# Kernel optimization log

Measured on AMD Instinct MI355X. Metric: run time of the kernel, lower is better.

The kernel has to match this reference:

```python
import jax, jax.numpy as jnp
import numpy as np

IN_FEATS, N_HIDDEN, NUM_LAYERS, N_CLASSES, CLS_HIDDEN = 166, 76, 2, 2, 510
T, N, E = 3, 100000, 1600000
RRELU_SLOPE = (1.0 / 8.0 + 1.0 / 3.0) / 2.0  # eval-mode RReLU = leaky relu with mean slope


def setup_inputs() -> dict:
    key = jax.random.key(0)
    ks = jax.random.split(key, 24)
    d = {}
    d['feats'] = jax.random.normal(ks[0], (T, N, IN_FEATS), jnp.float32)
    d['src'] = jax.random.randint(ks[1], (T, E), 0, N, jnp.int32)
    d['dst'] = jax.random.randint(ks[2], (T, E), 0, N, jnp.int32)
    # TopK scorers (uniform +-1/sqrt(feats))
    s0 = 1.0 / np.sqrt(IN_FEATS)
    s1 = 1.0 / np.sqrt(N_HIDDEN)
    d['scorer0'] = jax.random.uniform(ks[3], (IN_FEATS, 1), jnp.float32, -s0, s0)
    d['scorer1'] = jax.random.uniform(ks[4], (N_HIDDEN, 1), jnp.float32, -s1, s1)
    # GCN weights (xavier-ish)
    d['gcn_w0'] = jax.random.normal(ks[5], (IN_FEATS, N_HIDDEN), jnp.float32) * np.sqrt(2.0 / (IN_FEATS + N_HIDDEN))
    d['gcn_w1'] = jax.random.normal(ks[6], (N_HIDDEN, N_HIDDEN), jnp.float32) * np.sqrt(2.0 / (2 * N_HIDDEN))
    # GRU params, torch layout: W_ih [3H, H_in], W_hh [3H, H], gate order (r, z, n)
    g = 1.0 / np.sqrt(N_HIDDEN)
    H3 = 3 * N_HIDDEN
    d['gru0_wih'] = jax.random.uniform(ks[7], (H3, N_HIDDEN), jnp.float32, -g, g)
    d['gru0_whh'] = jax.random.uniform(ks[8], (H3, N_HIDDEN), jnp.float32, -g, g)
    d['gru0_bih'] = jax.random.uniform(ks[9], (H3,), jnp.float32, -g, g)
    d['gru0_bhh'] = jax.random.uniform(ks[10], (H3,), jnp.float32, -g, g)
    d['gru1_wih'] = jax.random.uniform(ks[11], (H3, N_HIDDEN), jnp.float32, -g, g)
    d['gru1_whh'] = jax.random.uniform(ks[12], (H3, N_HIDDEN), jnp.float32, -g, g)
    d['gru1_bih'] = jax.random.uniform(ks[13], (H3,), jnp.float32, -g, g)
    d['gru1_bhh'] = jax.random.uniform(ks[14], (H3,), jnp.float32, -g, g)
    # MLP
    m1 = 1.0 / np.sqrt(N_HIDDEN)
    m2 = 1.0 / np.sqrt(CLS_HIDDEN)
    d['mlp_w1'] = jax.random.uniform(ks[15], (N_HIDDEN, CLS_HIDDEN), jnp.float32, -m1, m1)
    d['mlp_b1'] = jax.random.uniform(ks[16], (CLS_HIDDEN,), jnp.float32, -m1, m1)
    d['mlp_w2'] = jax.random.uniform(ks[17], (CLS_HIDDEN, N_CLASSES), jnp.float32, -m2, m2)
    d['mlp_b2'] = jax.random.uniform(ks[18], (N_CLASSES,), jnp.float32, -m2, m2)
    return d


def _topk_pool(x, scorer, k):
    # x: [N, F]; returns X_tilde: [F, k]
    scores = (x @ scorer).ravel() / jnp.linalg.norm(scorer)
    vals, idx = jax.lax.top_k(scores, k)
    out = x[idx] * jnp.tanh(vals)[:, None]  # [k, F]
    return out.T


def _gru_step(x, h, wih, whh, bih, bhh):
    # x: [B, H_in], h: [B, H]; torch GRU gate order r, z, n
    gx = x @ wih.T + bih
    gh = h @ whh.T + bhh
    H = h.shape[1]
    rx, zx, nx = gx[:, :H], gx[:, H:2 * H], gx[:, 2 * H:]
    rh, zh, nh = gh[:, :H], gh[:, H:2 * H], gh[:, 2 * H:]
    r = jax.nn.sigmoid(rx + rh)
    z = jax.nn.sigmoid(zx + zh)
    n = jnp.tanh(nx + r * nh)
    return (1.0 - z) * n + z * h


def _graph_conv(x, W, src, dst, n_nodes):
    # DGL GraphConv, norm='both', bias=False, RReLU (eval) activation
    deg_out = jnp.zeros((n_nodes,), x.dtype).at[src].add(1.0)
    deg_in = jnp.zeros((n_nodes,), x.dtype).at[dst].add(1.0)
    norm_src = jnp.clip(deg_out, 1.0, None) ** -0.5
    norm_dst = jnp.clip(deg_in, 1.0, None) ** -0.5
    h = (x * norm_src[:, None]) @ W  # project first (small out dim)
    agg = jax.ops.segment_sum(h[src], dst, num_segments=n_nodes)
    out = agg * norm_dst[:, None]
    return jnp.where(out >= 0, out, out * RRELU_SLOPE)


def reference(feats, src, dst, scorer0, scorer1, gcn_w0, gcn_w1,
              gru0_wih, gru0_whh, gru0_bih, gru0_bhh,
              gru1_wih, gru1_whh, gru1_bih, gru1_bhh,
              mlp_w1, mlp_b1, mlp_w2, mlp_b2):
    scorers = [scorer0, scorer1]
    gcn_ws = [gcn_w0, gcn_w1]
    grus = [(gru0_wih, gru0_whh, gru0_bih, gru0_bhh),
            (gru1_wih, gru1_whh, gru1_bih, gru1_bhh)]
    feat_list = [feats[t] for t in range(T)]
    for i in range(NUM_LAYERS):
        W = gcn_ws[i]
        wih, whh, bih, bhh = grus[i]
        for t in range(T):
            x_tilde = _topk_pool(feat_list[t], scorers[i], N_HIDDEN)  # [F, k]
            W = _gru_step(x_tilde, W, wih, whh, bih, bhh)  # evolve weights
            feat_list[t] = _graph_conv(feat_list[t], W, src[t], dst[t], N)
    h = feat_list[-1]
    h = jax.nn.relu(h @ mlp_w1 + mlp_b1)
    return h @ mlp_w2 + mlp_b2
```

## Files before the change

kernel.cpp:

```cpp
#include <hip/hip_runtime.h>
#include <math.h>

#define NN 100000
#define EE 1600000
#define F0 166
#define HID 76
#define H3 228
#define CHID 510
#define SLOPE 0.22916666666666666f
#define CAND_MAX 4096
#define NBIN 4096
#define HPAD 20

#define BSH 9
#define BSZ 512
#define NBKT 196
#define CH 4096
#define NCHK 391

__device__ __forceinline__ unsigned f2key(float f){
    unsigned u = __float_as_uint(f);
    return (u & 0x80000000u) ? ~u : (u | 0x80000000u);
}
__device__ __forceinline__ float key2f(unsigned k){
    unsigned u = (k & 0x80000000u) ? (k & 0x7fffffffu) : ~k;
    return __uint_as_float(u);
}

__global__ void scorer_norms_k(const float* __restrict__ s0, const float* __restrict__ s1,
                               float* __restrict__ outn){
    __shared__ float red[256];
    int tid = threadIdx.x;
    float a = 0.f;
    for (int k = tid; k < F0; k += 256) a += s0[k]*s0[k];
    red[tid] = a; __syncthreads();
    for (int s = 128; s > 0; s >>= 1){ if (tid < s) red[tid] += red[tid+s]; __syncthreads(); }
    if (tid == 0) outn[0] = 1.0f/sqrtf(red[0]);
    __syncthreads();
    float b = 0.f;
    for (int k = tid; k < HID; k += 256) b += s1[k]*s1[k];
    red[tid] = b; __syncthreads();
    for (int s = 128; s > 0; s >>= 1){ if (tid < s) red[tid] += red[tid+s]; __syncthreads(); }
    if (tid == 0) outn[1] = 1.0f/sqrtf(red[0]);
}

__global__ void pad_k(const float* __restrict__ w1, const float* __restrict__ b1,
                      const float* __restrict__ w2, float* __restrict__ w1t,
                      float* __restrict__ b1p, float* __restrict__ w2p){
    int idx = blockIdx.x*256 + threadIdx.x;
    if (idx < 512*HID){
        int j = idx / HID, k = idx - j*HID;
        w1t[idx] = (j < CHID) ? w1[k*CHID + j] : 0.f;
    }
    if (idx < 512)  b1p[idx] = (idx < CHID)   ? b1[idx] : 0.f;
    if (idx < 1024) w2p[idx] = (idx < CHID*2) ? w2[idx] : 0.f;
}


__global__ __launch_bounds__(256) void p1_hist_k(const int* __restrict__ src, const int* __restrict__ dst,
                                                 int* __restrict__ bhS, int* __restrict__ bhD){
    __shared__ int hS[NBKT], hD[NBKT];
    int t = blockIdx.y, blk = blockIdx.x, tid = threadIdx.x;
    for (int i = tid; i < NBKT; i += 256){ hS[i] = 0; hD[i] = 0; }
    __syncthreads();
    size_t ebase = (size_t)t*EE + (size_t)blk*CH;
    int m = EE - blk*CH; if (m > CH) m = CH;
    for (int j = tid; j < m; j += 256){
        atomicAdd(&hS[src[ebase + j] >> BSH], 1);
        atomicAdd(&hD[dst[ebase + j] >> BSH], 1);
    }
    __syncthreads();
    for (int i = tid; i < NBKT; i += 256){
        bhS[((size_t)t*NBKT + i)*NCHK + blk] = hS[i];
        bhD[((size_t)t*NBKT + i)*NCHK + blk] = hD[i];
    }
}

__global__ __launch_bounds__(512) void p2_scan_k(int* __restrict__ bhS, int* __restrict__ bhD,
                                                 int* __restrict__ ctS, int* __restrict__ ctD){
    __shared__ int sd[512];
    int b = blockIdx.x, t = blockIdx.y, tid = threadIdx.x;
    for (int a = 0; a < 2; a++){
        int* bh = a ? bhD : bhS;
        int* ct = a ? ctD : ctS;
        int* row = bh + ((size_t)t*NBKT + b)*NCHK;
        int v = (tid < NCHK) ? row[tid] : 0;
        sd[tid] = v; __syncthreads();
        for (int off = 1; off < 512; off <<= 1){
            int x = (tid >= off) ? sd[tid - off] : 0;
            __syncthreads();
            sd[tid] += x;
            __syncthreads();
        }
        if (tid < NCHK) row[tid] = sd[tid] - v;
        if (tid == 511) ct[t*NBKT + b] = sd[511];
        __syncthreads();
    }
}

__global__ __launch_bounds__(256) void p3_base_k(const int* __restrict__ ctS, const int* __restrict__ ctD,
                                                 int* __restrict__ bbS, int* __restrict__ bbD){
    __shared__ int sd[256];
    int tid = threadIdx.x;
    for (int a = 0; a < 2; a++){
        const int* ct = a ? ctD : ctS;
        int* bb = a ? bbD : bbS;
        for (int t = 0; t < 3; t++){
            int v = (tid < NBKT) ? ct[t*NBKT + tid] : 0;
            sd[tid] = v; __syncthreads();
            for (int off = 1; off < 256; off <<= 1){
                int x = (tid >= off) ? sd[tid - off] : 0;
                __syncthreads();
                sd[tid] += x;
                __syncthreads();
            }
            if (tid < NBKT) bb[t*(NBKT+1) + tid] = sd[tid] - v;
            if (tid == 0)   bb[t*(NBKT+1) + NBKT] = EE;
            __syncthreads();
        }
    }
}

__global__ __launch_bounds__(256) void p4_scatter_k(const int* __restrict__ src, const int* __restrict__ dst,
                                                    const int* __restrict__ bhS, const int* __restrict__ bhD,
                                                    const int* __restrict__ bbS, const int* __restrict__ bbD,
                                                    int* __restrict__ srcpart,
                                                    unsigned long long* __restrict__ pairpart){
    __shared__ int baseS[NBKT], baseD[NBKT], cS[NBKT], cD[NBKT];
    int t = blockIdx.y, blk = blockIdx.x, tid = threadIdx.x;
    for (int i = tid; i < NBKT; i += 256){
        baseS[i] = bbS[t*(NBKT+1) + i] + bhS[((size_t)t*NBKT + i)*NCHK + blk];
        baseD[i] = bbD[t*(NBKT+1) + i] + bhD[((size_t)t*NBKT + i)*NCHK + blk];
        cS[i] = 0; cD[i] = 0;
    }
    __syncthreads();
    size_t ebase = (size_t)t*EE + (size_t)blk*CH;
    int m = EE - blk*CH; if (m > CH) m = CH;
    int* sp = srcpart + (size_t)t*EE;
    unsigned long long* pp = pairpart + (size_t)t*EE;
    for (int j = tid; j < m; j += 256){
        int s = src[ebase + j], d = dst[ebase + j];
        int bs = s >> BSH, bd = d >> BSH;
        int r0 = atomicAdd(&cS[bs], 1);
        sp[baseS[bs] + r0] = s;
        int r1 = atomicAdd(&cD[bd], 1);
        pp[baseD[bd] + r1] = ((unsigned long long)(unsigned)s << 32) | (unsigned)d;
    }
}

__global__ __launch_bounds__(256) void p5_degO_k(const int* __restrict__ srcpart,
                                                 const int* __restrict__ bbS,
                                                 int* __restrict__ degO){
    __shared__ int cnt[BSZ];
    int b = blockIdx.x, t = blockIdx.y, tid = threadIdx.x;
    for (int i = tid; i < BSZ; i += 256) cnt[i] = 0;
    __syncthreads();
    int st = bbS[t*(NBKT+1) + b], en = bbS[t*(NBKT+1) + b + 1];
    const int* sp = srcpart + (size_t)t*EE;
    for (int j = st + tid; j < en; j += 256) atomicAdd(&cnt[sp[j] & (BSZ-1)], 1);
    __syncthreads();
    int nb = b << BSH;
    for (int i = tid; i < BSZ; i += 256){
        int n = nb + i;
        if (n < NN) degO[t*NN + n] = cnt[i];
    }
}

__global__ __launch_bounds__(512) void p6_csr_k(const unsigned long long* __restrict__ pairpart,
                                                const int* __restrict__ bbD,
                                                int* __restrict__ degI, int* __restrict__ rs,
                                                int* __restrict__ col){
    __shared__ int cnt[BSZ];
    __shared__ int sc[BSZ];
    __shared__ int fc[BSZ];
    int b = blockIdx.x, t = blockIdx.y, tid = threadIdx.x;
    cnt[tid] = 0; fc[tid] = 0;
    __syncthreads();
    int st = bbD[t*(NBKT+1) + b], en = bbD[t*(NBKT+1) + b + 1];
    const unsigned long long* pp = pairpart + (size_t)t*EE;
    for (int j = st + tid; j < en; j += 512)
        atomicAdd(&cnt[(int)(pp[j] & (unsigned long long)(BSZ-1))], 1);
    __syncthreads();
    int v = cnt[tid];
    sc[tid] = v; __syncthreads();
    for (int off = 1; off < 512; off <<= 1){
        int x = (tid >= off) ? sc[tid - off] : 0;
        __syncthreads();
        sc[tid] += x;
        __syncthreads();
    }
    int ex = sc[tid] - v;
    int nb = b << BSH;
    int n = nb + tid;
    if (n < NN){ degI[t*NN + n] = v; rs[t*NN + n] = st + ex; }
    sc[tid] = ex;
    __syncthreads();
    int* ct = col + (size_t)t*EE;
    for (int j = st + tid; j < en; j += 512){
        unsigned long long p = pp[j];
        int d = (int)(p & 0xffffffffull);
        int li = d & (BSZ-1);
        int r = atomicAdd(&fc[li], 1);
        ct[st + sc[li] + r] = (int)(p >> 32);
    }
}


__global__ void norm_k(const int* __restrict__ degO, const int* __restrict__ degI,
                       float* __restrict__ nO, float* __restrict__ nI){
    int t = blockIdx.y;
    int n = blockIdx.x*256 + threadIdx.x;
    if (n < NN){
        int o = degO[t*NN + n]; if (o < 1) o = 1;
        int i = degI[t*NN + n]; if (i < 1) i = 1;
        nO[t*NN + n] = 1.0f/sqrtf((float)o);
        nI[t*NN + n] = 1.0f/sqrtf((float)i);
    }
}

template<int F, int PAD>
__global__ __launch_bounds__(256) void score_k(const float* __restrict__ x,
                                               const float* __restrict__ scorer,
                                               const float* __restrict__ invn,
                                               float* __restrict__ scores,
                                               unsigned* hist){
    __shared__ float xs[64*PAD];
    __shared__ float part[256];
    int tid = threadIdx.x;
    int n0 = blockIdx.x*64;
    int nodes = NN - n0; if (nodes > 64) nodes = 64;
    for (int idx = tid; idx < nodes*F; idx += 256){
        int n = idx / F, k = idx - n*F;
        xs[n*PAD + k] = x[(size_t)(n0+n)*F + k];
    }
    __syncthreads();
    int w = __builtin_amdgcn_readfirstlane(tid >> 6);
    int lane = tid & 63;
    int k0 = (F*w) >> 2, k1 = (F*(w+1)) >> 2;
    const float* xrow = xs + lane*PAD;
    float s = 0.f;
    for (int k = k0; k < k1; k++) s += xrow[k]*scorer[k];
    part[w*64 + lane] = s;
    __syncthreads();
    if (tid < 64 && n0 + tid < NN){
        float tot = (part[tid] + part[64+tid] + part[128+tid] + part[192+tid]) * invn[0];
        scores[n0 + tid] = tot;
        atomicAdd(&hist[f2key(tot) >> 20], 1u);
    }
}

__global__ void select_bin_k(const unsigned* __restrict__ hist, int* thr){
    __shared__ unsigned cs[256];
    int tid = threadIdx.x;
    unsigned s = 0;
    int base = NBIN - 1 - tid*16;
    for (int j = 0; j < 16; j++) s += hist[base - j];
    cs[tid] = s; __syncthreads();
    if (tid == 0){
        unsigned acc = 0; int c = 0;
        for (; c < 256; c++){ if (acc + cs[c] >= 76u) break; acc += cs[c]; }
        int b = NBIN - 1 - c*16;
        int sel = 0;
        for (int j = 0; j < 16; j++){
            acc += hist[b - j];
            if (acc >= 76u){ sel = b - j; break; }
        }
        *thr = sel;
    }
}

__global__ void compact_k(const float* __restrict__ scores, const int* __restrict__ thr,
                          float* __restrict__ cv, int* __restrict__ ci, int* cnt){
    int n = blockIdx.x*256 + threadIdx.x;
    if (n >= NN) return;
    float s = scores[n];
    if ((int)(f2key(s) >> 20) >= *thr){
        int p = atomicAdd(cnt, 1);
        if (p < CAND_MAX){ cv[p] = s; ci[p] = n; }
    }
}

__global__ __launch_bounds__(256) void topk_k(const float* __restrict__ cv,
                                              const int* __restrict__ ci,
                                              const int* __restrict__ cnt,
                                              int* __restrict__ topidx,
                                              float* __restrict__ tanhv){
    __shared__ unsigned long long keys[CAND_MAX];
    int tid = threadIdx.x;
    int M = *cnt; if (M > CAND_MAX) M = CAND_MAX;
    for (int i = tid; i < M; i += 256)
        keys[i] = ((unsigned long long)f2key(cv[i]) << 32) | (unsigned)(~ci[i]);
    __syncthreads();
    for (int i = tid; i < M; i += 256){
        unsigned long long ki = keys[i];
        int r = 0;
        for (int j = 0; j < M; j++) r += (keys[j] > ki) ? 1 : 0;
        if (r < 76){
            topidx[r] = (int)(~(unsigned)(ki & 0xffffffffu));
            tanhv[r]  = tanhf(key2f((unsigned)(ki >> 32)));
        }
    }
}

template<int F>
__global__ void gru_k(const float* __restrict__ cur, const int* __restrict__ topidx,
                      const float* __restrict__ tanhv, float* __restrict__ W,
                      float* __restrict__ Wt,
                      const float* __restrict__ wih, const float* __restrict__ whh,
                      const float* __restrict__ bih, const float* __restrict__ bhh){
    __shared__ float xr[HID], hr[HID], gx[H3], gh[H3];
    int r = blockIdx.x, tid = threadIdx.x;
    if (tid < HID){
        xr[tid] = cur[(size_t)topidx[tid]*F + r] * tanhv[tid];
        hr[tid] = W[r*HID + tid];
    }
    __syncthreads();
    if (tid < H3){
        const float* wi = wih + tid*HID;
        const float* wh = whh + tid*HID;
        float sa = 0.f, sb = 0.f;
        for (int k = 0; k < HID; k++){ sa += xr[k]*wi[k]; sb += hr[k]*wh[k]; }
        gx[tid] = bih[tid] + sa;
        gh[tid] = bhh[tid] + sb;
    }
    __syncthreads();
    if (tid < HID){
        float rr = 1.f/(1.f + expf(-(gx[tid] + gh[tid])));
        float zz = 1.f/(1.f + expf(-(gx[HID+tid] + gh[HID+tid])));
        float nn = tanhf(gx[2*HID+tid] + rr*gh[2*HID+tid]);
        float nv = (1.f - zz)*nn + zz*hr[tid];
        W[r*HID + tid] = nv;
        int c = tid >> 2, i = tid & 3;
        Wt[(c*F + r)*4 + i] = nv;
    }
}

template<int F, int PAD, int NB>
__global__ __launch_bounds__(256) void gemm_k(const float* __restrict__ x,
                                              const float* __restrict__ Wt,
                                              const float* __restrict__ nO,
                                              float* __restrict__ h){
    __shared__ __align__(16) float xs[NB*PAD];
    int tid = threadIdx.x;
    int n0 = blockIdx.x*NB;
    int nodes = NN - n0; if (nodes > NB) nodes = NB;
    for (int idx = tid; idx < nodes*F; idx += 256){
        int n = idx / F, k = idx - n*F;
        xs[n*PAD + k] = x[(size_t)(n0+n)*F + k];
    }
    __syncthreads();
    int w = __builtin_amdgcn_readfirstlane(tid >> 6);
    int lane = tid & 63;
    int c0 = w*5;
    const float4* Wt4 = (const float4*)Wt;
    float4 accA[5], accB[5];
    #pragma unroll
    for (int c = 0; c < 5; c++){
        accA[c] = make_float4(0.f,0.f,0.f,0.f);
        accB[c] = make_float4(0.f,0.f,0.f,0.f);
    }
    const float* xA = xs + lane*PAD;
    const float* xB = xs + ((NB==128) ? (lane+64)*PAD : lane*PAD);
    for (int k = 0; k < F; k++){
        float xa = xA[k];
        float xb = 0.f;
        if constexpr (NB == 128) xb = xB[k];
        #pragma unroll
        for (int c = 0; c < 5; c++){
            float4 wv = Wt4[(c0 + c)*F + k];
            accA[c].x += xa*wv.x; accA[c].y += xa*wv.y;
            accA[c].z += xa*wv.z; accA[c].w += xa*wv.w;
            if constexpr (NB == 128){
                accB[c].x += xb*wv.x; accB[c].y += xb*wv.y;
                accB[c].z += xb*wv.z; accB[c].w += xb*wv.w;
            }
        }
    }
    int nc = (w == 3) ? 4 : 5;
    int nA = n0 + lane;
    if (nA < NN){
        float nm = nO[nA];
        float4* h4 = (float4*)h + (size_t)nA*HPAD + c0;
        for (int c = 0; c < nc; c++){
            float4 a = accA[c];
            h4[c] = make_float4(a.x*nm, a.y*nm, a.z*nm, a.w*nm);
        }
    }
    if constexpr (NB == 128){
        int nB = n0 + 64 + lane;
        if (nB < NN){
            float nm = nO[nB];
            float4* h4 = (float4*)h + (size_t)nB*HPAD + c0;
            for (int c = 0; c < nc; c++){
                float4 a = accB[c];
                h4[c] = make_float4(a.x*nm, a.y*nm, a.z*nm, a.w*nm);
            }
        }
    }
}

__global__ void agg_k(const int* __restrict__ rs, const int* __restrict__ degI,
                      const int* __restrict__ col, const float* __restrict__ h,
                      const float* __restrict__ nI, float* __restrict__ ft){
    int idx = blockIdx.x*256 + threadIdx.x;
    if (idx >= NN*19) return;
    int n = idx/19, c = idx - n*19;
    int st = rs[n], cnt = degI[n];
    const float4* h4 = (const float4*)h;
    float ax=0.f, ay=0.f, az=0.f, aw=0.f;
    int e = 0;
    for (; e + 2 <= cnt; e += 2){
        int s0 = col[st + e];
        int s1 = col[st + e + 1];
        float4 v0 = h4[(size_t)s0*HPAD + c];
        float4 v1 = h4[(size_t)s1*HPAD + c];
        ax += v0.x + v1.x; ay += v0.y + v1.y;
        az += v0.z + v1.z; aw += v0.w + v1.w;
    }
    if (e < cnt){
        int s = col[st + e];
        float4 v = h4[(size_t)s*HPAD + c];
        ax += v.x; ay += v.y; az += v.z; aw += v.w;
    }
    float nm = nI[n];
    ax*=nm; ay*=nm; az*=nm; aw*=nm;
    ax = ax >= 0.f ? ax : ax*SLOPE;
    ay = ay >= 0.f ? ay : ay*SLOPE;
    az = az >= 0.f ? az : az*SLOPE;
    aw = aw >= 0.f ? aw : aw*SLOPE;
    ((float4*)ft)[(size_t)n*19 + c] = make_float4(ax,ay,az,aw);
}

__global__ __launch_bounds__(256) void mlp_k(const float* __restrict__ ft,
                                             const float* __restrict__ w1t,
                                             const float* __restrict__ b1p,
                                             const float* __restrict__ w2p,
                                             const float* __restrict__ b2,
                                             float* __restrict__ out){
    __shared__ __align__(16) float hs[128*HID];
    __shared__ float apA0[256], apA1[256], apB0[256], apB1[256];
    int tid = threadIdx.x;
    int n0 = blockIdx.x*128;
    int nodes = NN - n0; if (nodes > 128) nodes = 128;
    const float4* g4 = (const float4*)(ft + (size_t)n0*HID);
    float4* s4 = (float4*)hs;
    int lim = nodes*19;
    for (int idx = tid; idx < 128*19; idx += 256)
        s4[idx] = (idx < lim) ? g4[idx] : make_float4(0.f,0.f,0.f,0.f);
    __syncthreads();
    int w = __builtin_amdgcn_readfirstlane(tid >> 6);
    int lane = tid & 63;
    const float4* hA = (const float4*)(hs + lane*HID);
    const float4* hB = (const float4*)(hs + (lane+64)*HID);
    float aA0=0.f, aA1=0.f, aB0=0.f, aB1=0.f;
    for (int g = w; g < 128; g += 4){
        int j0 = g << 2;
        const float* wr = w1t + j0*HID;
        float b0 = b1p[j0], b1v = b1p[j0+1], b2v = b1p[j0+2], b3v = b1p[j0+3];
        float sA0=b0, sA1=b1v, sA2=b2v, sA3=b3v;
        float sB0=b0, sB1=b1v, sB2=b2v, sB3=b3v;
        #pragma unroll
        for (int k4 = 0; k4 < 19; k4++){
            float4 a = hA[k4];
            float4 b = hB[k4];
            int k = k4 << 2;
            float w00=wr[k],         w01=wr[k+1],         w02=wr[k+2],         w03=wr[k+3];
            float w10=wr[HID+k],     w11=wr[HID+k+1],     w12=wr[HID+k+2],     w13=wr[HID+k+3];
            float w20=wr[2*HID+k],   w21=wr[2*HID+k+1],   w22=wr[2*HID+k+2],   w23=wr[2*HID+k+3];
            float w30=wr[3*HID+k],   w31=wr[3*HID+k+1],   w32=wr[3*HID+k+2],   w33=wr[3*HID+k+3];
            sA0 += a.x*w00 + a.y*w01 + a.z*w02 + a.w*w03;
            sA1 += a.x*w10 + a.y*w11 + a.z*w12 + a.w*w13;
            sA2 += a.x*w20 + a.y*w21 + a.z*w22 + a.w*w23;
            sA3 += a.x*w30 + a.y*w31 + a.z*w32 + a.w*w33;
            sB0 += b.x*w00 + b.y*w01 + b.z*w02 + b.w*w03;
            sB1 += b.x*w10 + b.y*w11 + b.z*w12 + b.w*w13;
            sB2 += b.x*w20 + b.y*w21 + b.z*w22 + b.w*w23;
            sB3 += b.x*w30 + b.y*w31 + b.z*w32 + b.w*w33;
        }
        sA0 = fmaxf(sA0, 0.f); sA1 = fmaxf(sA1, 0.f);
        sA2 = fmaxf(sA2, 0.f); sA3 = fmaxf(sA3, 0.f);
        sB0 = fmaxf(sB0, 0.f); sB1 = fmaxf(sB1, 0.f);
        sB2 = fmaxf(sB2, 0.f); sB3 = fmaxf(sB3, 0.f);
        float u00 = w2p[j0*2],   u01 = w2p[j0*2+1];
        float u10 = w2p[j0*2+2], u11 = w2p[j0*2+3];
        float u20 = w2p[j0*2+4], u21 = w2p[j0*2+5];
        float u30 = w2p[j0*2+6], u31 = w2p[j0*2+7];
        aA0 += sA0*u00 + sA1*u10 + sA2*u20 + sA3*u30;
        aA1 += sA0*u01 + sA1*u11 + sA2*u21 + sA3*u31;
        aB0 += sB0*u00 + sB1*u10 + sB2*u20 + sB3*u30;
        aB1 += sB0*u01 + sB1*u11 + sB2*u21 + sB3*u31;
    }
    apA0[w*64 + lane] = aA0; apA1[w*64 + lane] = aA1;
    apB0[w*64 + lane] = aB0; apB1[w*64 + lane] = aB1;
    __syncthreads();
    if (tid < 64){
        int n = n0 + tid;
        if (n < NN){
            float r0 = apA0[tid] + apA0[64+tid] + apA0[128+tid] + apA0[192+tid] + b2[0];
            float r1 = apA1[tid] + apA1[64+tid] + apA1[128+tid] + apA1[192+tid] + b2[1];
            out[(size_t)n*2]   = r0;
            out[(size_t)n*2+1] = r1;
        }
    } else if (tid < 128){
        int l = tid - 64;
        int n = n0 + 64 + l;
        if (n < NN){
            float r0 = apB0[l] + apB0[64+l] + apB0[128+l] + apB0[192+l] + b2[0];
            float r1 = apB1[l] + apB1[64+l] + apB1[128+l] + apB1[192+l] + b2[1];
            out[(size_t)n*2]   = r0;
            out[(size_t)n*2+1] = r1;
        }
    }
}

extern "C" void kernel_launch(void* const* d_in, const int* in_sizes, int n_in,
                              void* d_out, int out_size, void* d_ws, size_t ws_size,
                              hipStream_t stream)
{
    (void)in_sizes; (void)n_in; (void)out_size; (void)ws_size;
    const float* feats   = (const float*)d_in[0];
    const int*   src     = (const int*)d_in[1];
    const int*   dst     = (const int*)d_in[2];
    const float* scorer0 = (const float*)d_in[3];
    const float* scorer1 = (const float*)d_in[4];
    const float* gcnw[2] = {(const float*)d_in[5],  (const float*)d_in[6]};
    const float* wih[2]  = {(const float*)d_in[7],  (const float*)d_in[11]};
    const float* whh[2]  = {(const float*)d_in[8],  (const float*)d_in[12]};
    const float* bih[2]  = {(const float*)d_in[9],  (const float*)d_in[13]};
    const float* bhh[2]  = {(const float*)d_in[10], (const float*)d_in[14]};
    const float* w1 = (const float*)d_in[15];
    const float* b1 = (const float*)d_in[16];
    const float* w2 = (const float*)d_in[17];
    const float* b2 = (const float*)d_in[18];
    float* out = (float*)d_out;

    char* p = (char*)d_ws;
    auto alloc = [&](size_t bytes) -> void* {
        void* r = (void*)p;
        p += (bytes + 255) & ~(size_t)255;
        return r;
    };
    float* ft[3];
    for (int t = 0; t < 3; t++) ft[t] = (float*)alloc((size_t)NN*HID*4);
    float* hbuf    = (float*)alloc((size_t)NN*HPAD*16);
    int*   col_all = (int*)alloc((size_t)3*EE*4);
    float* nO_all  = (float*)alloc((size_t)3*NN*4);
    float* nI_all  = (float*)alloc((size_t)3*NN*4);
    int*   rs_all  = (int*)alloc((size_t)3*NN*4);
    int*   dO_all  = (int*)alloc((size_t)3*NN*4);
    int*   dI_all  = (int*)alloc((size_t)3*NN*4);
    int* srcpart = (int*)alloc((size_t)3*EE*4);
    unsigned long long* pairpart = (unsigned long long*)alloc((size_t)3*EE*8);
    int* bhS = (int*)alloc((size_t)3*NBKT*NCHK*4);
    int* bhD = (int*)alloc((size_t)3*NBKT*NCHK*4);
    int* ctS = (int*)alloc((size_t)3*NBKT*4);
    int* ctD = (int*)alloc((size_t)3*NBKT*4);
    int* bbS = (int*)alloc((size_t)3*(NBKT+1)*4);
    int* bbD = (int*)alloc((size_t)3*(NBKT+1)*4);

    float*    scores = (float*)alloc((size_t)NN*4);
    float*    cv     = (float*)alloc(CAND_MAX*4);
    int*      ci     = (int*)alloc(CAND_MAX*4);
    int*      thr    = (int*)alloc(256);
    int*      topidx = (int*)alloc(128*4);
    float*    tanhv  = (float*)alloc(128*4);
    float*    Wbuf   = (float*)alloc((size_t)F0*HID*4 + 256);
    float*    Wt     = (float*)alloc((size_t)19*F0*16 + 4096);
    float*    invn   = (float*)alloc(256);
    float*    w1t    = (float*)alloc((size_t)512*HID*4);
    float*    b1p    = (float*)alloc(512*4);
    float*    w2p    = (float*)alloc(1024*4);

    char* zbase = p;
    unsigned* hist6 = (unsigned*)alloc((size_t)6*NBIN*4);
    int*      ccnt6 = (int*)alloc(6*256);
    size_t zsize = (size_t)(p - zbase);

    const int gN  = (NN + 255)/256;
    const int gA  = (NN*19 + 255)/256;
    const int gB  = (NN + 63)/64;
    const int gB2 = (NN + 127)/128;
    const int gP  = (512*HID + 255)/256;

    hipMemsetAsync(zbase, 0, zsize, stream);
    scorer_norms_k<<<1,256,0,stream>>>(scorer0, scorer1, invn);
    pad_k<<<gP,256,0,stream>>>(w1, b1, w2, w1t, b1p, w2p);

    p1_hist_k<<<dim3(NCHK,3),256,0,stream>>>(src, dst, bhS, bhD);
    p2_scan_k<<<dim3(NBKT,3),512,0,stream>>>(bhS, bhD, ctS, ctD);
    p3_base_k<<<1,256,0,stream>>>(ctS, ctD, bbS, bbD);
    p4_scatter_k<<<dim3(NCHK,3),256,0,stream>>>(src, dst, bhS, bhD, bbS, bbD, srcpart, pairpart);
    p5_degO_k<<<dim3(NBKT,3),256,0,stream>>>(srcpart, bbS, dO_all);
    p6_csr_k<<<dim3(NBKT,3),512,0,stream>>>(pairpart, bbD, dI_all, rs_all, col_all);
    norm_k<<<dim3(gN,3),256,0,stream>>>(dO_all, dI_all, nO_all, nI_all);

    for (int i = 0; i < 2; i++){
        hipMemcpyAsync(Wbuf, gcnw[i], (size_t)((i==0)?F0:HID)*HID*4, hipMemcpyDeviceToDevice, stream);
        for (int t = 0; t < 3; t++){
            int q = i*3 + t;
            unsigned* hist = hist6 + (size_t)q*NBIN;
            int* ccnt = ccnt6 + q*64;
            const float* cur = (i == 0) ? (feats + (size_t)t*NN*F0) : ft[t];
            if (i == 0) score_k<F0,167><<<gB,256,0,stream>>>(cur, scorer0, invn+0, scores, hist);
            else        score_k<HID,77><<<gB,256,0,stream>>>(cur, scorer1, invn+1, scores, hist);
            select_bin_k<<<1,256,0,stream>>>(hist, thr);
            compact_k<<<gN,256,0,stream>>>(scores, thr, cv, ci, ccnt);
            topk_k<<<1,256,0,stream>>>(cv, ci, ccnt, topidx, tanhv);
            if (i == 0){
                gru_k<F0><<<F0,256,0,stream>>>(cur, topidx, tanhv, Wbuf, Wt, wih[i], whh[i], bih[i], bhh[i]);
                gemm_k<F0,167,64><<<gB,256,0,stream>>>(cur, Wt, nO_all + (size_t)t*NN, hbuf);
            } else {
                gru_k<HID><<<HID,256,0,stream>>>(cur, topidx, tanhv, Wbuf, Wt, wih[i], whh[i], bih[i], bhh[i]);
                gemm_k<HID,77,128><<<gB2,256,0,stream>>>(cur, Wt, nO_all + (size_t)t*NN, hbuf);
            }
            agg_k<<<gA,256,0,stream>>>(rs_all + (size_t)t*NN, dI_all + (size_t)t*NN,
                                       col_all + (size_t)t*EE, hbuf, nI_all + (size_t)t*NN, ft[t]);
        }
    }

    mlp_k<<<gB2,256,0,stream>>>(ft[2], w1t, b1p, w2p, b2, out);
}
```

Measured before the change: 2.558 ms.

## Fuse norm and select kernels, unroll aggregation, restructure MLP with split-J atomics

Norm computation moves into the degree and CSR kernels, and threshold selection moves into every compact block, which removes two launches per stage. The aggregation gather loop is unrolled to four edges to keep more loads in flight. The MLP is rewritten so that each thread holds one node row in registers, W1 slices are staged in shared memory, and the hidden dimension is split across two blocks whose partial outputs are combined with atomics into a zeroed output. The MLP change adds register pressure, a memset, atomics and nondeterministic summation order, and every compact block now recomputes the histogram selection.

After: 2.587 ms. No clear change (+1.1%).

```diff
diff --git a/kernel.cpp b/kernel.cpp
--- a/kernel.cpp
+++ b/kernel.cpp
@@ -11,6 +11,7 @@
 #define CAND_MAX 4096
 #define NBIN 4096
 #define HPAD 20
+#define MJ 256
 
 #define BSH 9
 #define BSZ 512
@@ -150,7 +151,7 @@
 
 __global__ __launch_bounds__(256) void p5_degO_k(const int* __restrict__ srcpart,
                                                  const int* __restrict__ bbS,
-                                                 int* __restrict__ degO){
+                                                 float* __restrict__ nO){
     __shared__ int cnt[BSZ];
     int b = blockIdx.x, t = blockIdx.y, tid = threadIdx.x;
     for (int i = tid; i < BSZ; i += 256) cnt[i] = 0;
@@ -162,13 +163,17 @@
     int nb = b << BSH;
     for (int i = tid; i < BSZ; i += 256){
         int n = nb + i;
-        if (n < NN) degO[t*NN + n] = cnt[i];
+        if (n < NN){
+            int o = cnt[i]; if (o < 1) o = 1;
+            nO[t*NN + n] = 1.0f/sqrtf((float)o);
+        }
     }
 }
 
 __global__ __launch_bounds__(512) void p6_csr_k(const unsigned long long* __restrict__ pairpart,
                                                 const int* __restrict__ bbD,
                                                 int* __restrict__ degI, int* __restrict__ rs,
+                                                float* __restrict__ nI,
                                                 int* __restrict__ col){
     __shared__ int cnt[BSZ];
     __shared__ int sc[BSZ];
@@ -192,7 +197,12 @@
     int ex = sc[tid] - v;
     int nb = b << BSH;
     int n = nb + tid;
-    if (n < NN){ degI[t*NN + n] = v; rs[t*NN + n] = st + ex; }
+    if (n < NN){
+        degI[t*NN + n] = v;
+        rs[t*NN + n] = st + ex;
+        int ii = v; if (ii < 1) ii = 1;
+        nI[t*NN + n] = 1.0f/sqrtf((float)ii);
+    }
     sc[tid] = ex;
     __syncthreads();
     int* ct = col + (size_t)t*EE;
@@ -205,18 +215,6 @@
     }
 }
 
-
-__global__ void norm_k(const int* __restrict__ degO, const int* __restrict__ degI,
-                       float* __restrict__ nO, float* __restrict__ nI){
-    int t = blockIdx.y;
-    int n = blockIdx.x*256 + threadIdx.x;
-    if (n < NN){
-        int o = degO[t*NN + n]; if (o < 1) o = 1;
-        int i = degI[t*NN + n]; if (i < 1) i = 1;
-        nO[t*NN + n] = 1.0f/sqrtf((float)o);
-        nI[t*NN + n] = 1.0f/sqrtf((float)i);
-    }
-}
 
 template<int F, int PAD>
 __global__ __launch_bounds__(256) void score_k(const float* __restrict__ x,
@@ -249,8 +247,11 @@
     }
 }
 
-__global__ void select_bin_k(const unsigned* __restrict__ hist, int* thr){
+__global__ __launch_bounds__(256) void compact_k(const float* __restrict__ scores,
+                                                 const unsigned* __restrict__ hist,
+                                                 float* __restrict__ cv, int* __restrict__ ci, int* cnt){
     __shared__ unsigned cs[256];
+    __shared__ int thr_s;
     int tid = threadIdx.x;
     unsigned s = 0;
     int base = NBIN - 1 - tid*16;
@@ -265,18 +266,16 @@
             acc += hist[b - j];
             if (acc >= 76u){ sel = b - j; break; }
         }
-        *thr = sel;
-    }
-}
-
-__global__ void compact_k(const float* __restrict__ scores, const int* __restrict__ thr,
-                          float* __restrict__ cv, int* __restrict__ ci, int* cnt){
-    int n = blockIdx.x*256 + threadIdx.x;
+        thr_s = sel;
+    }
+    __syncthreads();
+    int thr = thr_s;
+    int n = blockIdx.x*256 + tid;
     if (n >= NN) return;
-    float s = scores[n];
-    if ((int)(f2key(s) >> 20) >= *thr){
+    float sv = scores[n];
+    if ((int)(f2key(sv) >> 20) >= thr){
         int p = atomicAdd(cnt, 1);
-        if (p < CAND_MAX){ cv[p] = s; ci[p] = n; }
+        if (p < CAND_MAX){ cv[p] = sv; ci[p] = n; }
     }
 }
 
@@ -409,15 +408,21 @@
     const float4* h4 = (const float4*)h;
     float ax=0.f, ay=0.f, az=0.f, aw=0.f;
     int e = 0;
-    for (; e + 2 <= cnt; e += 2){
+    for (; e + 4 <= cnt; e += 4){
         int s0 = col[st + e];
         int s1 = col[st + e + 1];
+        int s2 = col[st + e + 2];
+        int s3 = col[st + e + 3];
         float4 v0 = h4[(size_t)s0*HPAD + c];
         float4 v1 = h4[(size_t)s1*HPAD + c];
-        ax += v0.x + v1.x; ay += v0.y + v1.y;
-        az += v0.z + v1.z; aw += v0.w + v1.w;
-    }
-    if (e < cnt){
+        float4 v2 = h4[(size_t)s2*HPAD + c];
+        float4 v3 = h4[(size_t)s3*HPAD + c];
+        ax += (v0.x + v1.x) + (v2.x + v3.x);
+        ay += (v0.y + v1.y) + (v2.y + v3.y);
+        az += (v0.z + v1.z) + (v2.z + v3.z);
+        aw += (v0.w + v1.w) + (v2.w + v3.w);
+    }
+    for (; e < cnt; e++){
         int s = col[st + e];
         float4 v = h4[(size_t)s*HPAD + c];
         ax += v.x; ay += v.y; az += v.z; aw += v.w;
@@ -431,86 +436,55 @@
     ((float4*)ft)[(size_t)n*19 + c] = make_float4(ax,ay,az,aw);
 }
 
-__global__ __launch_bounds__(256) void mlp_k(const float* __restrict__ ft,
-                                             const float* __restrict__ w1t,
-                                             const float* __restrict__ b1p,
-                                             const float* __restrict__ w2p,
-                                             const float* __restrict__ b2,
-                                             float* __restrict__ out){
-    __shared__ __align__(16) float hs[128*HID];
-    __shared__ float apA0[256], apA1[256], apB0[256], apB1[256];
-    int tid = threadIdx.x;
-    int n0 = blockIdx.x*128;
-    int nodes = NN - n0; if (nodes > 128) nodes = 128;
-    const float4* g4 = (const float4*)(ft + (size_t)n0*HID);
-    float4* s4 = (float4*)hs;
-    int lim = nodes*19;
-    for (int idx = tid; idx < 128*19; idx += 256)
-        s4[idx] = (idx < lim) ? g4[idx] : make_float4(0.f,0.f,0.f,0.f);
-    __syncthreads();
-    int w = __builtin_amdgcn_readfirstlane(tid >> 6);
-    int lane = tid & 63;
-    const float4* hA = (const float4*)(hs + lane*HID);
-    const float4* hB = (const float4*)(hs + (lane+64)*HID);
-    float aA0=0.f, aA1=0.f, aB0=0.f, aB1=0.f;
-    for (int g = w; g < 128; g += 4){
-        int j0 = g << 2;
-        const float* wr = w1t + j0*HID;
-        float b0 = b1p[j0], b1v = b1p[j0+1], b2v = b1p[j0+2], b3v = b1p[j0+3];
-        float sA0=b0, sA1=b1v, sA2=b2v, sA3=b3v;
-        float sB0=b0, sB1=b1v, sB2=b2v, sB3=b3v;
+__global__ __launch_bounds__(1024) void mlp2_k(const float* __restrict__ ft,
+                                               const float* __restrict__ w1t,
+                                               const float* __restrict__ b1p,
+                                               const float* __restrict__ w2p,
+                                               const float* __restrict__ b2,
+                                               float* __restrict__ out){
+    __shared__ __align__(16) float ws[MJ*HID];
+    __shared__ float w2s[MJ*2];
+    __shared__ float b1s[MJ];
+    int tid = threadIdx.x;
+    int jbase = blockIdx.y * MJ;
+    const float4* wg = (const float4*)(w1t + (size_t)jbase*HID);
+    float4* wsv = (float4*)ws;
+    for (int i = tid; i < MJ*HID/4; i += 1024) wsv[i] = wg[i];
+    if (tid < MJ*2) w2s[tid] = w2p[jbase*2 + tid];
+    if (tid < MJ)   b1s[tid] = b1p[jbase + tid];
+    __syncthreads();
+    int node = blockIdx.x*1024 + tid;
+    if (node >= NN) return;
+    float4 r[19];
+    const float4* rp = (const float4*)(ft + (size_t)node*HID);
+    #pragma unroll
+    for (int k = 0; k < 19; k++) r[k] = rp[k];
+    float acc0 = 0.f, acc1 = 0.f;
+    if (jbase == 0){ acc0 = b2[0]; acc1 = b2[1]; }
+    const float4* ws4 = (const float4*)ws;
+    for (int g = 0; g < MJ/4; g++){
+        int j0 = g*4;
+        float s0 = b1s[j0], s1 = b1s[j0+1], s2 = b1s[j0+2], s3 = b1s[j0+3];
+        const float4* wr = ws4 + j0*19;
         #pragma unroll
         for (int k4 = 0; k4 < 19; k4++){
-            float4 a = hA[k4];
-            float4 b = hB[k4];
-            int k = k4 << 2;
-            float w00=wr[k],         w01=wr[k+1],         w02=wr[k+2],         w03=wr[k+3];
-            float w10=wr[HID+k],     w11=wr[HID+k+1],     w12=wr[HID+k+2],     w13=wr[HID+k+3];
-            float w20=wr[2*HID+k],   w21=wr[2*HID+k+1],   w22=wr[2*HID+k+2],   w23=wr[2*HID+k+3];
-            float w30=wr[3*HID+k],   w31=wr[3*HID+k+1],   w32=wr[3*HID+k+2],   w33=wr[3*HID+k+3];
-            sA0 += a.x*w00 + a.y*w01 + a.z*w02 + a.w*w03;
-            sA1 += a.x*w10 + a.y*w11 + a.z*w12 + a.w*w13;
-            sA2 += a.x*w20 + a.y*w21 + a.z*w22 + a.w*w23;
-            sA3 += a.x*w30 + a.y*w31 + a.z*w32 + a.w*w33;
-            sB0 += b.x*w00 + b.y*w01 + b.z*w02 + b.w*w03;
-            sB1 += b.x*w10 + b.y*w11 + b.z*w12 + b.w*w13;
-            sB2 += b.x*w20 + b.y*w21 + b.z*w22 + b.w*w23;
-            sB3 += b.x*w30 + b.y*w31 + b.z*w32 + b.w*w33;
-        }
-        sA0 = fmaxf(sA0, 0.f); sA1 = fmaxf(sA1, 0.f);
-        sA2 = fmaxf(sA2, 0.f); sA3 = fmaxf(sA3, 0.f);
-        sB0 = fmaxf(sB0, 0.f); sB1 = fmaxf(sB1, 0.f);
-        sB2 = fmaxf(sB2, 0.f); sB3 = fmaxf(sB3, 0.f);
-        float u00 = w2p[j0*2],   u01 = w2p[j0*2+1];
-        float u10 = w2p[j0*2+2], u11 = w2p[j0*2+3];
-        float u20 = w2p[j0*2+4], u21 = w2p[j0*2+5];
-        float u30 = w2p[j0*2+6], u31 = w2p[j0*2+7];
-        aA0 += sA0*u00 + sA1*u10 + sA2*u20 + sA3*u30;
-        aA1 += sA0*u01 + sA1*u11 + sA2*u21 + sA3*u31;
-        aB0 += sB0*u00 + sB1*u10 + sB2*u20 + sB3*u30;
-        aB1 += sB0*u01 + sB1*u11 + sB2*u21 + sB3*u31;
-    }
-    apA0[w*64 + lane] = aA0; apA1[w*64 + lane] = aA1;
-    apB0[w*64 + lane] = aB0; apB1[w*64 + lane] = aB1;
-    __syncthreads();
-    if (tid < 64){
-        int n = n0 + tid;
-        if (n < NN){
-            float r0 = apA0[tid] + apA0[64+tid] + apA0[128+tid] + apA0[192+tid] + b2[0];
-            float r1 = apA1[tid] + apA1[64+tid] + apA1[128+tid] + apA1[192+tid] + b2[1];
-            out[(size_t)n*2]   = r0;
-            out[(size_t)n*2+1] = r1;
-        }
-    } else if (tid < 128){
-        int l = tid - 64;
-        int n = n0 + 64 + l;
-        if (n < NN){
-            float r0 = apB0[l] + apB0[64+l] + apB0[128+l] + apB0[192+l] + b2[0];
-            float r1 = apB1[l] + apB1[64+l] + apB1[128+l] + apB1[192+l] + b2[1];
-            out[(size_t)n*2]   = r0;
-            out[(size_t)n*2+1] = r1;
-        }
-    }
+            float4 rv = r[k4];
+            float4 w0 = wr[k4];
+            float4 w1 = wr[19 + k4];
+            float4 w2v = wr[38 + k4];
+            float4 w3 = wr[57 + k4];
+            s0 += rv.x*w0.x + rv.y*w0.y + rv.z*w0.z + rv.w*w0.w;
+            s1 += rv.x*w1.x + rv.y*w1.y + rv.z*w1.z + rv.w*w1.w;
+            s2 += rv.x*w2v.x + rv.y*w2v.y + rv.z*w2v.z + rv.w*w2v.w;
+            s3 += rv.x*w3.x + rv.y*w3.y + rv.z*w3.z + rv.w*w3.w;
+        }
+        s0 = fmaxf(s0, 0.f); s1 = fmaxf(s1, 0.f);
+        s2 = fmaxf(s2, 0.f); s3 = fmaxf(s3, 0.f);
+        acc0 += s0*w2s[j0*2]   + s1*w2s[j0*2+2] + s2*w2s[j0*2+4] + s3*w2s[j0*2+6];
+        acc1 += s0*w2s[j0*2+1] + s1*w2s[j0*2+3] + s2*w2s[j0*2+5] + s3*w2s[j0*2+7];
+    }
+    atomicAdd(&out[(size_t)node*2],     acc0);
+    atomicAdd(&out[(size_t)node*2 + 1], acc1);
 }
 
 extern "C" void kernel_launch(void* const* d_in, const int* in_sizes, int n_in,
@@ -547,7 +521,6 @@
     float* nO_all  = (float*)alloc((size_t)3*NN*4);
     float* nI_all  = (float*)alloc((size_t)3*NN*4);
     int*   rs_all  = (int*)alloc((size_t)3*NN*4);
-    int*   dO_all  = (int*)alloc((size_t)3*NN*4);
     int*   dI_all  = (int*)alloc((size_t)3*NN*4);
     int* srcpart = (int*)alloc((size_t)3*EE*4);
     unsigned long long* pairpart = (unsigned long long*)alloc((size_t)3*EE*8);
@@ -561,7 +534,6 @@
     float*    scores = (float*)alloc((size_t)NN*4);
     float*    cv     = (float*)alloc(CAND_MAX*4);
     int*      ci     = (int*)alloc(CAND_MAX*4);
-    int*      thr    = (int*)alloc(256);
     int*      topidx = (int*)alloc(128*4);
     float*    tanhv  = (float*)alloc(128*4);
     float*    Wbuf   = (float*)alloc((size_t)F0*HID*4 + 256);
@@ -580,9 +552,11 @@
     const int gA  = (NN*19 + 255)/256;
     const int gB  = (NN + 63)/64;
     const int gB2 = (NN + 127)/128;
+    const int gM  = (NN + 1023)/1024;
     const int gP  = (512*HID + 255)/256;
 
     hipMemsetAsync(zbase, 0, zsize, stream);
+    hipMemsetAsync(out, 0, (size_t)NN*2*4, stream);
     scorer_norms_k<<<1,256,0,stream>>>(scorer0, scorer1, invn);
     pad_k<<<gP,256,0,stream>>>(w1, b1, w2, w1t, b1p, w2p);
 
@@ -590,9 +564,8 @@
     p2_scan_k<<<dim3(NBKT,3),512,0,stream>>>(bhS, bhD, ctS, ctD);
     p3_base_k<<<1,256,0,stream>>>(ctS, ctD, bbS, bbD);
     p4_scatter_k<<<dim3(NCHK,3),256,0,stream>>>(src, dst, bhS, bhD, bbS, bbD, srcpart, pairpart);
-    p5_degO_k<<<dim3(NBKT,3),256,0,stream>>>(srcpart, bbS, dO_all);
-    p6_csr_k<<<dim3(NBKT,3),512,0,stream>>>(pairpart, bbD, dI_all, rs_all, col_all);
-    norm_k<<<dim3(gN,3),256,0,stream>>>(dO_all, dI_all, nO_all, nI_all);
+    p5_degO_k<<<dim3(NBKT,3),256,0,stream>>>(srcpart, bbS, nO_all);
+    p6_csr_k<<<dim3(NBKT,3),512,0,stream>>>(pairpart, bbD, dI_all, rs_all, nI_all, col_all);
 
     for (int i = 0; i < 2; i++){
         hipMemcpyAsync(Wbuf, gcnw[i], (size_t)((i==0)?F0:HID)*HID*4, hipMemcpyDeviceToDevice, stream);
@@ -603,8 +576,7 @@
             const float* cur = (i == 0) ? (feats + (size_t)t*NN*F0) : ft[t];
             if (i == 0) score_k<F0,167><<<gB,256,0,stream>>>(cur, scorer0, invn+0, scores, hist);
             else        score_k<HID,77><<<gB,256,0,stream>>>(cur, scorer1, invn+1, scores, hist);
-            select_bin_k<<<1,256,0,stream>>>(hist, thr);
-            compact_k<<<gN,256,0,stream>>>(scores, thr, cv, ci, ccnt);
+            compact_k<<<gN,256,0,stream>>>(scores, hist, cv, ci, ccnt);
             topk_k<<<1,256,0,stream>>>(cv, ci, ccnt, topidx, tanhv);
             if (i == 0){
                 gru_k<F0><<<F0,256,0,stream>>>(cur, topidx, tanhv, Wbuf, Wt, wih[i], whh[i], bih[i], bhh[i]);
@@ -618,5 +590,5 @@
         }
     }
 
-    mlp_k<<<gB2,256,0,stream>>>(ft[2], w1t, b1p, w2p, b2, out);
-}
+    mlp2_k<<<dim3(gM,2),1024,0,stream>>>(ft[2], w1t, b1p, w2p, b2, out);
+}
```
